# Performance work log

Hardware: AMD Instinct MI355X
Metric: run time of the kernel (lower is better)

Reference implementation:

```python
import jax, jax.numpy as jnp
import numpy as np

B, C, D, L, H = 128, 1000, 300, 40, 100


def setup_inputs() -> dict:
    key = jax.random.key(0)
    ks = jax.random.split(key, 16)
    def rn(i, shape, sc=1.0):
        return (jax.random.normal(ks[i], shape, jnp.float32) * sc).astype(jnp.float32)
    return {
        "utt": rn(0, (B, L, D)),
        "sys_slots": rn(1, (B, D), 0.1),
        "conf_slots": rn(2, (B, D), 0.1),
        "conf_values": rn(3, (B, D), 0.1),
        "y_past_state": jax.random.uniform(ks[4], (B, C), jnp.float32),
        "slot_emb": rn(5, (C, D), 0.1),
        "value_emb": rn(6, (C, D), 0.1),
        "Wc": rn(7, (D, 2 * D), 0.05), "bc": jnp.zeros((D,), jnp.float32),
        "conv_w1": rn(8, (D, D, 1), 0.05), "conv_b1": jnp.zeros((D,), jnp.float32),
        "conv_w2": rn(9, (D, D, 2), 0.05), "conv_b2": jnp.zeros((D,), jnp.float32),
        "conv_w3": rn(10, (D, D, 3), 0.05), "conv_b3": jnp.zeros((D,), jnp.float32),
        "Wd": rn(11, (H, D), 0.05), "bd": jnp.zeros((H,), jnp.float32),
        "Wmr": rn(12, (H, D), 0.05), "bmr": jnp.zeros((H,), jnp.float32),
        "Wmc": rn(13, (H, D), 0.05), "bmc": jnp.zeros((H,), jnp.float32),
        "Wj": rn(14, (1, H), 0.05), "bj": jnp.zeros((1,), jnp.float32),
    }


def _conv_relu_pool(x_ncl, w, b):
    # x_ncl: [B, D, L]; w: [F, D, k] -> relu(conv) then global max-pool over time -> [B, F]
    y = jax.lax.conv_general_dilated(x_ncl, w, (1,), 'VALID',
                                     dimension_numbers=('NCH', 'OIH', 'NCH'))
    y = jax.nn.relu(y + b[None, :, None])
    return jnp.max(y, axis=2)


def _sig_linear(x, W, b):
    # Sequential(Sigmoid, Linear): Linear applied to sigmoid(x)
    return jax.nn.sigmoid(x) @ W.T + b


def reference(utt, sys_slots, conf_slots, conf_values, y_past_state,
              slot_emb, value_emb, Wc, bc,
              conv_w1, conv_b1, conv_w2, conv_b2, conv_w3, conv_b3,
              Wd, bd, Wmr, bmr, Wmc, bmc, Wj, bj):
    # CNN utterance encoder: sum of 3 conv branches (filter widths 1,2,3)
    x = jnp.transpose(utt, (0, 2, 1))  # [B, D, L]
    final_utt = (_conv_relu_pool(x, conv_w1, conv_b1)
                 + _conv_relu_pool(x, conv_w2, conv_b2)
                 + _conv_relu_pool(x, conv_w3, conv_b3))  # [B, D]

    # candidates_transform = sigmoid(Linear(cat(slot_emb, value_emb)))
    cand = jax.nn.sigmoid(jnp.concatenate([slot_emb, value_emb], axis=1) @ Wc.T + bc)  # [C, D]

    # fused version of the per-batch repeat/addcmul loop: [B, C, D]
    contrib = cand[None, :, :] * final_utt[:, None, :]

    y1 = _sig_linear(_sig_linear(contrib, Wd, bd), Wj, bj)  # [B, C, 1]

    # system-act request gate: ([C,D]@[D,B]) @ [B,D] -> [C, D]
    m_r = (slot_emb @ sys_slots.T) @ final_utt
    y2 = _sig_linear(_sig_linear(m_r, Wmr, bmr), Wj, bj)  # [C, 1]

    # system-act confirm gate
    m_c = ((slot_emb @ conf_slots.T) * (value_emb @ conf_values.T)) @ final_utt  # [C, D]
    y3 = _sig_linear(_sig_linear(m_c, Wmc, bmc), Wj, bj)  # [C, 1]

    y_presoftmax = y1 + y2[None, :, :] + y3[None, :, :]  # [B, C, 1]
    combine = 0.5
    return combine * y_presoftmax[..., 0] + (1.0 - combine) * y_past_state  # [B, C]
```

## Files before the change

### kernel.cpp

```cpp
#include <hip/hip_runtime.h>
#include <hip/hip_bf16.h>

#define OFF_Y23     0
#define OFF_BDP     4096
#define OFF_WJP     4544
#define OFF_BCP     4992
#define OFF_BMRP    6272
#define OFF_BMCP    6720
#define OFF_WALLT   7168
#define OFF_PBF     1235968
#define OFF_FUBF    20896768
#define OFF_FUBFT   20978688
#define OFF_CATSV   21060608
#define OFF_WCPK    22371328
#define OFF_CANDBF  22780928
#define OFF_WDFRAG  23436288
#define OFF_WMRFRAG 23507968
#define OFF_WMCFRAG 23579648
#define OFF_SYSB    23651328
#define OFF_CONFSB  23733248
#define OFF_CONFVB  23815168
#define OFF_PRBF    23897088
#define OFF_PCBF    24159232
#define OFF_SMRBF   24421376
#define OFF_SMCBF   25076736
#define OFF_XBF     25732096

typedef short bf16x8_t __attribute__((ext_vector_type(8)));
typedef float f32x4_t  __attribute__((ext_vector_type(4)));

__device__ __forceinline__ float sigmoidf_fast(float x) {
    return __builtin_amdgcn_rcpf(1.0f + __expf(-x));
}
__device__ __forceinline__ unsigned short f2bf(float x) {
    unsigned int u = __float_as_uint(x);
    unsigned int r = (u + 0x7FFFu + ((u >> 16) & 1u)) >> 16;
    return (unsigned short)r;
}
__device__ __forceinline__ float bf2f(unsigned short h) {
    return __uint_as_float(((unsigned int)h) << 16);
}

__device__ __forceinline__ float frag_fetch(const float* __restrict__ W, int i) {
    int entry = i >> 3, e = i & 7;
    int kt = entry / 448;
    int r = entry - kt * 448;
    int ni = r >> 6, lane = r & 63;
    int j = ni * 16 + (lane & 15);
    int k = kt * 32 + (lane >> 4) * 8 + e;
    return (j < 100 && k < 300) ? W[j * 300 + k] : 0.0f;
}

__global__ void pack_kernel(const float* __restrict__ w1, const float* __restrict__ w2,
                            const float* __restrict__ w3, const float* __restrict__ Wc,
                            const float* __restrict__ Wd, const float* __restrict__ Wmr,
                            const float* __restrict__ Wmc, const float* __restrict__ sys,
                            const float* __restrict__ confs, const float* __restrict__ confv,
                            const float* __restrict__ bd, const float* __restrict__ Wj,
                            const float* __restrict__ bmr, const float* __restrict__ bmc,
                            const float* __restrict__ bc, const float* __restrict__ slot,
                            const float* __restrict__ value, const float* __restrict__ utt,
                            unsigned short* __restrict__ WallTbf,
                            unsigned short* __restrict__ WdFrag,
                            unsigned short* __restrict__ WmrFrag,
                            unsigned short* __restrict__ WmcFrag,
                            float* __restrict__ bdPad, float* __restrict__ WjPad,
                            float* __restrict__ bmrPad, float* __restrict__ bmcPad,
                            float* __restrict__ bcPad,
                            unsigned short* __restrict__ sysB,
                            unsigned short* __restrict__ confsB,
                            unsigned short* __restrict__ confvB,
                            unsigned short* __restrict__ catsv,
                            unsigned short* __restrict__ WcPk,
                            unsigned short* __restrict__ Xbf) {
    int idx = blockIdx.x * blockDim.x + threadIdx.x;
    if (idx < 614400) {
        int tap = idx / 102400;
        int rem = idx - tap * 102400;
        int f = rem / 320, k = rem % 320;
        float v = 0.0f;
        if (f < 300 && k < 300) {
            int fd = f * 300 + k;
            if (tap == 0)      v = w1[fd];
            else if (tap == 1) v = w2[fd * 2 + 0];
            else if (tap == 2) v = w2[fd * 2 + 1];
            else               v = w3[fd * 3 + (tap - 3)];
        }
        WallTbf[idx] = f2bf(v);
    } else if (idx < 650240) {
        int i = idx - 614400;
        WdFrag[i] = f2bf(frag_fetch(Wd, i));
    } else if (idx < 686080) {
        int i = idx - 650240;
        WmrFrag[i] = f2bf(frag_fetch(Wmr, i));
    } else if (idx < 721920) {
        int i = idx - 686080;
        WmcFrag[i] = f2bf(frag_fetch(Wmc, i));
    } else if (idx < 722032) {
        int j = idx - 721920; bdPad[j] = (j < 100) ? bd[j] : 0.0f;
    } else if (idx < 722144) {
        int j = idx - 722032; WjPad[j] = (j < 100) ? Wj[j] : 0.0f;
    } else if (idx < 722256) {
        int j = idx - 722144; bmrPad[j] = (j < 100) ? bmr[j] : 0.0f;
    } else if (idx < 722368) {
        int j = idx - 722256; bmcPad[j] = (j < 100) ? bmc[j] : 0.0f;
    } else if (idx < 722688) {
        int j = idx - 722368; bcPad[j] = (j < 300) ? bc[j] : 0.0f;
    } else if (idx < 845568) {
        int i = idx - 722688;
        int m = i / 40960, r = i % 40960;
        int b = r / 320, k = r % 320;
        const float* src = (m == 0) ? sys : ((m == 1) ? confs : confv);
        unsigned short* dst = (m == 0) ? sysB : ((m == 1) ? confsB : confvB);
        dst[r] = f2bf((k < 300) ? src[b * 300 + k] : 0.0f);
    } else if (idx < 1500928) {
        int i = idx - 845568;
        int c = i / 640, k = i % 640;
        float v = 0.0f;
        if (c < 1000) {
            if (k < 300)                   v = slot[c * 300 + k];
            else if (k >= 320 && k < 620)  v = value[c * 300 + (k - 320)];
        }
        catsv[i] = f2bf(v);
    } else if (idx < 1705728) {
        int i = idx - 1500928;
        int f = i / 640, k = i % 640;
        float v = 0.0f;
        if (f < 300) {
            if (k < 300)                   v = Wc[f * 600 + k];
            else if (k >= 320 && k < 620)  v = Wc[f * 600 + 300 + (k - 320)];
        }
        WcPk[i] = f2bf(v);
    } else if (idx < 3344128) {
        int i = idx - 1705728;
        int m = i / 320, k = i % 320;
        Xbf[i] = f2bf((k < 300) ? utt[m * 300 + k] : 0.0f);
    }
}

__global__ __launch_bounds__(256) void early_kernel(
        const unsigned short* __restrict__ Xbf, const unsigned short* __restrict__ WallTbf,
        unsigned short* __restrict__ Pbf,
        const unsigned short* __restrict__ catsv, const unsigned short* __restrict__ WcPk,
        const float* __restrict__ bcPad, unsigned short* __restrict__ candbf,
        const unsigned short* __restrict__ sysB, const unsigned short* __restrict__ confsB,
        const unsigned short* __restrict__ confvB,
        unsigned short* __restrict__ Prbf, unsigned short* __restrict__ Pcbf) {
    __shared__ __attribute__((aligned(16))) char smem[40960];
    const int bid = blockIdx.x;
    const int tid = threadIdx.x;
    const int lane = tid & 63, w = tid >> 6;
    const int ln = lane & 15, lq = lane >> 4;

    if (bid < 600) {
        short* As = (short*)smem;
        short* Bs = (short*)(smem + 10240);
        const int m0 = (bid / 15) * 128;
        const int n0 = (bid % 15) * 128;
        const int wrow = w >> 1, wcol = w & 1;
        f32x4_t acc[4][4];
        #pragma unroll
        for (int i = 0; i < 4; i++)
            #pragma unroll
            for (int j = 0; j < 4; j++) acc[i][j] = (f32x4_t){0.f, 0.f, 0.f, 0.f};
        for (int kk = 0; kk < 320; kk += 32) {
            #pragma unroll
            for (int i = tid; i < 512; i += 256) {
                int row = i >> 2, q = i & 3;
                *(uint4*)(&As[row * 40 + q * 8]) =
                    *(const uint4*)(Xbf + (m0 + row) * 320 + kk + q * 8);
            }
            #pragma unroll
            for (int i = tid; i < 512; i += 256) {
                int row = i >> 2, q = i & 3;
                *(uint4*)(&Bs[row * 40 + q * 8]) =
                    *(const uint4*)(WallTbf + (n0 + row) * 320 + kk + q * 8);
            }
            __syncthreads();
            bf16x8_t a[4], b[4];
            #pragma unroll
            for (int mi = 0; mi < 4; mi++)
                a[mi] = *(const bf16x8_t*)(&As[(wrow * 64 + mi * 16 + ln) * 40 + lq * 8]);
            #pragma unroll
            for (int ni = 0; ni < 4; ni++)
                b[ni] = *(const bf16x8_t*)(&Bs[(wcol * 64 + ni * 16 + ln) * 40 + lq * 8]);
            #pragma unroll
            for (int mi = 0; mi < 4; mi++)
                #pragma unroll
                for (int ni = 0; ni < 4; ni++)
                    acc[mi][ni] = __builtin_amdgcn_mfma_f32_16x16x32_bf16(a[mi], b[ni], acc[mi][ni], 0, 0, 0);
            __syncthreads();
        }
        #pragma unroll
        for (int mi = 0; mi < 4; mi++) {
            #pragma unroll
            for (int ni = 0; ni < 4; ni++) {
                int col = n0 + wcol * 64 + ni * 16 + ln;
                #pragma unroll
                for (int reg = 0; reg < 4; reg++) {
                    int row = m0 + wrow * 64 + mi * 16 + lq * 4 + reg;
                    Pbf[row * 1920 + col] = f2bf(acc[mi][ni][reg]);
                }
            }
        }
    } else if (bid < 680) {
        short* As = (short*)smem;
        short* Bs = (short*)(smem + 5120);
        const int idx2 = bid - 600;
        const int m0 = (idx2 / 5) * 64, n0 = (idx2 % 5) * 64;
        const int wr = w & 1, wc = w >> 1;
        f32x4_t acc[2][2];
        #pragma unroll
        for (int i = 0; i < 2; i++)
            #pragma unroll
            for (int j = 0; j < 2; j++) acc[i][j] = (f32x4_t){0.f, 0.f, 0.f, 0.f};
        const int srow = tid >> 2, sq = tid & 3;
        for (int kk = 0; kk < 640; kk += 32) {
            *(uint4*)(&As[srow * 40 + sq * 8]) = *(const uint4*)(catsv + (m0 + srow) * 640 + kk + sq * 8);
            *(uint4*)(&Bs[srow * 40 + sq * 8]) = *(const uint4*)(WcPk  + (n0 + srow) * 640 + kk + sq * 8);
            __syncthreads();
            bf16x8_t a[2], b[2];
            #pragma unroll
            for (int mi = 0; mi < 2; mi++)
                a[mi] = *(const bf16x8_t*)(&As[(wr * 32 + mi * 16 + ln) * 40 + lq * 8]);
            #pragma unroll
            for (int ni = 0; ni < 2; ni++)
                b[ni] = *(const bf16x8_t*)(&Bs[(wc * 32 + ni * 16 + ln) * 40 + lq * 8]);
            #pragma unroll
            for (int mi = 0; mi < 2; mi++)
                #pragma unroll
                for (int ni = 0; ni < 2; ni++)
                    acc[mi][ni] = __builtin_amdgcn_mfma_f32_16x16x32_bf16(a[mi], b[ni], acc[mi][ni], 0, 0, 0);
            __syncthreads();
        }
        #pragma unroll
        for (int mi = 0; mi < 2; mi++) {
            #pragma unroll
            for (int ni = 0; ni < 2; ni++) {
                int n = n0 + wc * 32 + ni * 16 + ln;
                float bcv = bcPad[n];
                #pragma unroll
                for (int reg = 0; reg < 4; reg++) {
                    int cr = m0 + wr * 32 + mi * 16 + lq * 4 + reg;
                    candbf[cr * 320 + n] = f2bf(sigmoidf_fast(acc[mi][ni][reg] + bcv));
                }
            }
        }
    } else {
        short* As0 = (short*)smem;
        short* As1 = (short*)(smem + 5120);
        short* Bs0 = (short*)(smem + 10240);
        short* Bs1 = (short*)(smem + 20480);
        short* Bs2 = (short*)(smem + 30720);
        const int c0 = (bid - 680) * 64;
        f32x4_t accR[8], accS[8], accV[8];
        #pragma unroll
        for (int i = 0; i < 8; i++) {
            accR[i] = (f32x4_t){0.f, 0.f, 0.f, 0.f};
            accS[i] = (f32x4_t){0.f, 0.f, 0.f, 0.f};
            accV[i] = (f32x4_t){0.f, 0.f, 0.f, 0.f};
        }
        for (int kk = 0; kk < 320; kk += 32) {
            #pragma unroll
            for (int i = tid; i < 512; i += 256) {
                int mat = i >> 8, r2 = i & 255;
                int row = r2 >> 2, q = r2 & 3;
                short* dst = mat ? As1 : As0;
                *(uint4*)(&dst[row * 40 + q * 8]) =
                    *(const uint4*)(catsv + (c0 + row) * 640 + mat * 320 + kk + q * 8);
            }
            #pragma unroll
            for (int i = tid; i < 1536; i += 256) {
                int mat = i >> 9, r2 = i & 511;
                int row = r2 >> 2, q = r2 & 3;
                const unsigned short* src = (mat == 0) ? sysB : ((mat == 1) ? confsB : confvB);
                short* dst = (mat == 0) ? Bs0 : ((mat == 1) ? Bs1 : Bs2);
                *(uint4*)(&dst[row * 40 + q * 8]) =
                    *(const uint4*)(src + row * 320 + kk + q * 8);
            }
            __syncthreads();
            bf16x8_t aS = *(const bf16x8_t*)(&As0[(w * 16 + ln) * 40 + lq * 8]);
            bf16x8_t aV = *(const bf16x8_t*)(&As1[(w * 16 + ln) * 40 + lq * 8]);
            #pragma unroll
            for (int ni = 0; ni < 8; ni++) {
                bf16x8_t bR = *(const bf16x8_t*)(&Bs0[(ni * 16 + ln) * 40 + lq * 8]);
                bf16x8_t bS = *(const bf16x8_t*)(&Bs1[(ni * 16 + ln) * 40 + lq * 8]);
                bf16x8_t bV = *(const bf16x8_t*)(&Bs2[(ni * 16 + ln) * 40 + lq * 8]);
                accR[ni] = __builtin_amdgcn_mfma_f32_16x16x32_bf16(aS, bR, accR[ni], 0, 0, 0);
                accS[ni] = __builtin_amdgcn_mfma_f32_16x16x32_bf16(aS, bS, accS[ni], 0, 0, 0);
                accV[ni] = __builtin_amdgcn_mfma_f32_16x16x32_bf16(aV, bV, accV[ni], 0, 0, 0);
            }
            __syncthreads();
        }
        #pragma unroll
        for (int ni = 0; ni < 8; ni++) {
            int b = ni * 16 + ln;
            #pragma unroll
            for (int reg = 0; reg < 4; reg++) {
                int c = c0 + w * 16 + lq * 4 + reg;
                Prbf[c * 128 + b] = f2bf(accR[ni][reg]);
                Pcbf[c * 128 + b] = f2bf(accS[ni][reg] * accV[ni][reg]);
            }
        }
    }
}

__global__ __launch_bounds__(64) void combine_kernel(const unsigned short* __restrict__ Pbf,
        const float* __restrict__ b1, const float* __restrict__ b2,
        const float* __restrict__ b3, unsigned short* __restrict__ fubf,
        unsigned short* __restrict__ fubfT) {
    int b = blockIdx.x;
    int f = blockIdx.y * 64 + threadIdx.x;
    if (f >= 300) { fubf[b * 320 + f] = 0; fubfT[f * 128 + b] = 0; return; }
    const unsigned short* base = Pbf + (size_t)b * 40 * 1920;
    float m1 = -1e30f, m2 = -1e30f, m3 = -1e30f;
    float p1prev = 0.f, p3prev = 0.f, p3prev2 = 0.f, p4prev = 0.f;
    for (int t = 0; t < 40; ++t) {
        const unsigned short* r = base + t * 1920;
        float p0 = bf2f(r[f]);
        float p1 = bf2f(r[320 + f]);
        float p2 = bf2f(r[640 + f]);
        float p3 = bf2f(r[960 + f]);
        float p4 = bf2f(r[1280 + f]);
        float p5 = bf2f(r[1600 + f]);
        m1 = fmaxf(m1, p0);
        if (t >= 1) m2 = fmaxf(m2, p1prev + p2);
        if (t >= 2) m3 = fmaxf(m3, p3prev2 + p4prev + p5);
        p3prev2 = p3prev; p3prev = p3; p4prev = p4; p1prev = p1;
    }
    float r = fmaxf(m1 + b1[f], 0.f) + fmaxf(m2 + b2[f], 0.f) + fmaxf(m3 + b3[f], 0.f);
    unsigned short rb = f2bf(r);
    fubf[b * 320 + f]  = rb;
    fubfT[f * 128 + b] = rb;
}

__global__ __launch_bounds__(256) void mgate_gemm(const unsigned short* __restrict__ Prbf,
        const unsigned short* __restrict__ Pcbf, const unsigned short* __restrict__ fubfT,
        unsigned short* __restrict__ smrbf, unsigned short* __restrict__ smcbf) {
    __shared__ __attribute__((aligned(16))) short As[2][64 * 40];
    __shared__ __attribute__((aligned(16))) short Bs[64 * 40];
    const int tid = threadIdx.x;
    const int m0 = blockIdx.x * 64, n0 = blockIdx.y * 64;
    const int lane = tid & 63, w = tid >> 6;
    const int wr = w & 1, wc = w >> 1;
    const int ln = lane & 15, lq = lane >> 4;
    f32x4_t accR[2][2], accC[2][2];
    #pragma unroll
    for (int i = 0; i < 2; i++)
        #pragma unroll
        for (int j = 0; j < 2; j++) {
            accR[i][j] = (f32x4_t){0.f, 0.f, 0.f, 0.f};
            accC[i][j] = (f32x4_t){0.f, 0.f, 0.f, 0.f};
        }
    for (int kk = 0; kk < 128; kk += 32) {
        #pragma unroll
        for (int i = tid; i < 512; i += 256) {
            int mat = i >> 8, r2 = i & 255;
            int row = r2 >> 2, q = r2 & 3;
            const unsigned short* src = mat ? Pcbf : Prbf;
            *(uint4*)(&As[mat][row * 40 + q * 8]) =
                *(const uint4*)(src + (m0 + row) * 128 + kk + q * 8);
        }
        if (tid < 256) {
            int row = tid >> 2, q = tid & 3;
            *(uint4*)(&Bs[row * 40 + q * 8]) =
                *(const uint4*)(fubfT + (n0 + row) * 128 + kk + q * 8);
        }
        __syncthreads();
        bf16x8_t aR[2], aC[2], b[2];
        #pragma unroll
        for (int mi = 0; mi < 2; mi++) {
            aR[mi] = *(const bf16x8_t*)(&As[0][(wr * 32 + mi * 16 + ln) * 40 + lq * 8]);
            aC[mi] = *(const bf16x8_t*)(&As[1][(wr * 32 + mi * 16 + ln) * 40 + lq * 8]);
        }
        #pragma unroll
        for (int ni = 0; ni < 2; ni++)
            b[ni] = *(const bf16x8_t*)(&Bs[(wc * 32 + ni * 16 + ln) * 40 + lq * 8]);
        #pragma unroll
        for (int mi = 0; mi < 2; mi++)
            #pragma unroll
            for (int ni = 0; ni < 2; ni++) {
                accR[mi][ni] = __builtin_amdgcn_mfma_f32_16x16x32_bf16(aR[mi], b[ni], accR[mi][ni], 0, 0, 0);
                accC[mi][ni] = __builtin_amdgcn_mfma_f32_16x16x32_bf16(aC[mi], b[ni], accC[mi][ni], 0, 0, 0);
            }
        __syncthreads();
    }
    #pragma unroll
    for (int mi = 0; mi < 2; mi++) {
        #pragma unroll
        for (int ni = 0; ni < 2; ni++) {
            int f = n0 + wc * 32 + ni * 16 + ln;
            #pragma unroll
            for (int reg = 0; reg < 4; reg++) {
                int c = m0 + wr * 32 + mi * 16 + lq * 4 + reg;
                smrbf[c * 320 + f] = f2bf(sigmoidf_fast(accR[mi][ni][reg]));
                smcbf[c * 320 + f] = f2bf(sigmoidf_fast(accC[mi][ni][reg]));
            }
        }
    }
}

__global__ __launch_bounds__(256) void ygate_gemm(const unsigned short* __restrict__ smrbf,
        const unsigned short* __restrict__ smcbf, const unsigned short* __restrict__ WmrFrag,
        const unsigned short* __restrict__ WmcFrag, const float* __restrict__ bmrPad,
        const float* __restrict__ bmcPad, const float* __restrict__ WjPad,
        const float* __restrict__ bj, float* __restrict__ y23) {
    __shared__ __attribute__((aligned(16))) short As[2][64 * 40];
    __shared__ __attribute__((aligned(16))) short Bs[2][3584];
    const int tid = threadIdx.x;
    const int c0 = blockIdx.x * 64;
    const int lane = tid & 63, w = tid >> 6;
    const int ln = lane & 15, lq = lane >> 4;
    f32x4_t accR[7], accC[7];
    #pragma unroll
    for (int i = 0; i < 7; i++) {
        accR[i] = (f32x4_t){0.f, 0.f, 0.f, 0.f};
        accC[i] = (f32x4_t){0.f, 0.f, 0.f, 0.f};
    }
    for (int kt = 0; kt < 10; kt++) {
        int kk = kt * 32;
        #pragma unroll
        for (int i = tid; i < 512; i += 256) {
            int mat = i >> 8, r2 = i & 255;
            int row = r2 >> 2, q = r2 & 3;
            const unsigned short* src = mat ? smcbf : smrbf;
            *(uint4*)(&As[mat][row * 40 + q * 8]) =
                *(const uint4*)(src + (c0 + row) * 320 + kk + q * 8);
        }
        #pragma unroll
        for (int i = tid; i < 896; i += 256) {
            int mat = i / 448, j = i - mat * 448;
            const uint4* s = (const uint4*)((mat ? WmcFrag : WmrFrag) + kt * 3584);
            ((uint4*)&Bs[mat][0])[j] = s[j];
        }
        __syncthreads();
        bf16x8_t aR = *(const bf16x8_t*)(&As[0][(w * 16 + ln) * 40 + lq * 8]);
        bf16x8_t aC = *(const bf16x8_t*)(&As[1][(w * 16 + ln) * 40 + lq * 8]);
        #pragma unroll
        for (int ni = 0; ni < 7; ni++) {
            bf16x8_t bR = *(const bf16x8_t*)(&Bs[0][(ni * 64 + lane) * 8]);
            bf16x8_t bC = *(const bf16x8_t*)(&Bs[1][(ni * 64 + lane) * 8]);
            accR[ni] = __builtin_amdgcn_mfma_f32_16x16x32_bf16(aR, bR, accR[ni], 0, 0, 0);
            accC[ni] = __builtin_amdgcn_mfma_f32_16x16x32_bf16(aC, bC, accC[ni], 0, 0, 0);
        }
        __syncthreads();
    }
    float psum[4] = {0.f, 0.f, 0.f, 0.f};
    #pragma unroll
    for (int ni = 0; ni < 7; ni++) {
        int n = ni * 16 + ln;
        float wj = WjPad[n], br = bmrPad[n], bcv = bmcPad[n];
        #pragma unroll
        for (int reg = 0; reg < 4; reg++) {
            float hr = sigmoidf_fast(accR[ni][reg] + br);
            float hc = sigmoidf_fast(accC[ni][reg] + bcv);
            psum[reg] += (hr + hc) * wj;
        }
    }
    #pragma unroll
    for (int reg = 0; reg < 4; reg++) {
        float v = psum[reg];
        v += __shfl_xor(v, 1);
        v += __shfl_xor(v, 2);
        v += __shfl_xor(v, 4);
        v += __shfl_xor(v, 8);
        if (ln == 0) {
            int c = c0 + w * 16 + lq * 4 + reg;
            y23[c] = v + 2.0f * bj[0];
        }
    }
}

__global__ __launch_bounds__(256) void gemm2_kernel(const unsigned short* __restrict__ candbf,
        const unsigned short* __restrict__ fubf, const unsigned short* __restrict__ WdFrag,
        const float* __restrict__ bdPad, const float* __restrict__ WjPad,
        const float* __restrict__ bj, const float* __restrict__ y23,
        const float* __restrict__ ypast, float* __restrict__ out) {
    __shared__ __attribute__((aligned(16))) short Bs[2][3584];
    __shared__ float bdS[112], WjS[112], ybuf[128];
    const int c = blockIdx.x;
    const int tid = threadIdx.x;
    const int lane = tid & 63, w = tid >> 6;
    const int ln = lane & 15, lq = lane >> 4;
    if (tid < 112) { bdS[tid] = bdPad[tid]; WjS[tid] = WjPad[tid]; }

    const unsigned short* candRow = candbf + c * 320;
    const unsigned short* fuR0 = fubf + (w * 32 + ln) * 320;
    const unsigned short* fuR1 = fuR0 + 16 * 320;

    f32x4_t acc[2][7];
    #pragma unroll
    for (int mi = 0; mi < 2; mi++)
        #pragma unroll
        for (int ni = 0; ni < 7; ni++) acc[mi][ni] = (f32x4_t){0.f, 0.f, 0.f, 0.f};

    {
        const uint4* src = (const uint4*)(WdFrag);
        uint4* dst = (uint4*)&Bs[0][0];
        dst[tid] = src[tid];
        if (tid < 192) dst[tid + 256] = src[tid + 256];
    }
    __syncthreads();

    #pragma unroll
    for (int kt = 0; kt < 10; kt++) {
        if (kt < 9) {
            const uint4* src = (const uint4*)(WdFrag + (kt + 1) * 3584);
            uint4* dst = (uint4*)&Bs[(kt + 1) & 1][0];
            dst[tid] = src[tid];
            if (tid < 192) dst[tid + 256] = src[tid + 256];
        }
        const int k0 = kt * 32 + lq * 8;
        bf16x8_t cf  = *(const bf16x8_t*)(candRow + k0);
        bf16x8_t f0v = *(const bf16x8_t*)(fuR0 + k0);
        bf16x8_t f1v = *(const bf16x8_t*)(fuR1 + k0);
        bf16x8_t a0, a1;
        #pragma unroll
        for (int e = 0; e < 8; e += 2) {
            float cv0 = bf2f((unsigned short)cf[e]);
            float cv1 = bf2f((unsigned short)cf[e + 1]);
            float2 s0 = make_float2(sigmoidf_fast(cv0 * bf2f((unsigned short)f0v[e])),
                                    sigmoidf_fast(cv1 * bf2f((unsigned short)f0v[e + 1])));
            float2 s1 = make_float2(sigmoidf_fast(cv0 * bf2f((unsigned short)f1v[e])),
                                    sigmoidf_fast(cv1 * bf2f((unsigned short)f1v[e + 1])));
            __hip_bfloat162 p0 = __float22bfloat162_rn(s0);
            __hip_bfloat162 p1 = __float22bfloat162_rn(s1);
            ((unsigned int*)&a0)[e >> 1] = *(unsigned int*)&p0;
            ((unsigned int*)&a1)[e >> 1] = *(unsigned int*)&p1;
        }
        #pragma unroll
        for (int ni = 0; ni < 7; ni++) {
            bf16x8_t bfr = *(const bf16x8_t*)(&Bs[kt & 1][(ni * 64 + lane) * 8]);
            acc[0][ni] = __builtin_amdgcn_mfma_f32_16x16x32_bf16(a0, bfr, acc[0][ni], 0, 0, 0);
            acc[1][ni] = __builtin_amdgcn_mfma_f32_16x16x32_bf16(a1, bfr, acc[1][ni], 0, 0, 0);
        }
        __syncthreads();
    }

    float psum[2][4] = {{0.f, 0.f, 0.f, 0.f}, {0.f, 0.f, 0.f, 0.f}};
    #pragma unroll
    for (int mi = 0; mi < 2; mi++) {
        #pragma unroll
        for (int ni = 0; ni < 7; ni++) {
            int n = ni * 16 + ln;
            float bdv = bdS[n], wjv = WjS[n];
            #pragma unroll
            for (int reg = 0; reg < 4; reg++) {
                float h = sigmoidf_fast(acc[mi][ni][reg] + bdv);
                psum[mi][reg] += h * wjv;
            }
        }
    }
    #pragma unroll
    for (int mi = 0; mi < 2; mi++) {
        #pragma unroll
        for (int reg = 0; reg < 4; reg++) {
            float v = psum[mi][reg];
            v += __shfl_xor(v, 1);
            v += __shfl_xor(v, 2);
            v += __shfl_xor(v, 4);
            v += __shfl_xor(v, 8);
            if (ln == 0) ybuf[w * 32 + mi * 16 + lq * 4 + reg] = v;
        }
    }
    __syncthreads();
    if (tid < 128) {
        int b = tid;
        float y1 = ybuf[b] + bj[0];
        out[b * 1000 + c] = 0.5f * (y1 + y23[c]) + 0.5f * ypast[b * 1000 + c];
    }
}

extern "C" void kernel_launch(void* const* d_in, const int* in_sizes, int n_in,
                              void* d_out, int out_size, void* d_ws, size_t ws_size,
                              hipStream_t stream) {
    const float* utt   = (const float*)d_in[0];
    const float* sys   = (const float*)d_in[1];
    const float* confs = (const float*)d_in[2];
    const float* confv = (const float*)d_in[3];
    const float* ypast = (const float*)d_in[4];
    const float* slot  = (const float*)d_in[5];
    const float* value = (const float*)d_in[6];
    const float* Wc    = (const float*)d_in[7];
    const float* bc    = (const float*)d_in[8];
    const float* w1    = (const float*)d_in[9];
    const float* b1    = (const float*)d_in[10];
    const float* w2    = (const float*)d_in[11];
    const float* b2    = (const float*)d_in[12];
    const float* w3    = (const float*)d_in[13];
    const float* b3    = (const float*)d_in[14];
    const float* Wd    = (const float*)d_in[15];
    const float* bd    = (const float*)d_in[16];
    const float* Wmr   = (const float*)d_in[17];
    const float* bmr   = (const float*)d_in[18];
    const float* Wmc   = (const float*)d_in[19];
    const float* bmc   = (const float*)d_in[20];
    const float* Wj    = (const float*)d_in[21];
    const float* bj    = (const float*)d_in[22];

    char* wsb = (char*)d_ws;
    float* y23    = (float*)(wsb + OFF_Y23);
    float* bdPad  = (float*)(wsb + OFF_BDP);
    float* WjPad  = (float*)(wsb + OFF_WJP);
    float* bcPad  = (float*)(wsb + OFF_BCP);
    float* bmrPad = (float*)(wsb + OFF_BMRP);
    float* bmcPad = (float*)(wsb + OFF_BMCP);
    unsigned short* WallTbf = (unsigned short*)(wsb + OFF_WALLT);
    unsigned short* Pbf     = (unsigned short*)(wsb + OFF_PBF);
    unsigned short* fubf    = (unsigned short*)(wsb + OFF_FUBF);
    unsigned short* fubfT   = (unsigned short*)(wsb + OFF_FUBFT);
    unsigned short* catsv   = (unsigned short*)(wsb + OFF_CATSV);
    unsigned short* WcPk    = (unsigned short*)(wsb + OFF_WCPK);
    unsigned short* candbf  = (unsigned short*)(wsb + OFF_CANDBF);
    unsigned short* WdFrag  = (unsigned short*)(wsb + OFF_WDFRAG);
    unsigned short* WmrFrag = (unsigned short*)(wsb + OFF_WMRFRAG);
    unsigned short* WmcFrag = (unsigned short*)(wsb + OFF_WMCFRAG);
    unsigned short* sysB    = (unsigned short*)(wsb + OFF_SYSB);
    unsigned short* confsB  = (unsigned short*)(wsb + OFF_CONFSB);
    unsigned short* confvB  = (unsigned short*)(wsb + OFF_CONFVB);
    unsigned short* Prbf    = (unsigned short*)(wsb + OFF_PRBF);
    unsigned short* Pcbf    = (unsigned short*)(wsb + OFF_PCBF);
    unsigned short* smrbf   = (unsigned short*)(wsb + OFF_SMRBF);
    unsigned short* smcbf   = (unsigned short*)(wsb + OFF_SMCBF);
    unsigned short* Xbf     = (unsigned short*)(wsb + OFF_XBF);
    float* out = (float*)d_out;

    pack_kernel<<<13063, 256, 0, stream>>>(w1, w2, w3, Wc, Wd, Wmr, Wmc, sys, confs, confv,
                                           bd, Wj, bmr, bmc, bc, slot, value, utt,
                                           WallTbf, WdFrag, WmrFrag, WmcFrag,
                                           bdPad, WjPad, bmrPad, bmcPad, bcPad,
                                           sysB, confsB, confvB, catsv, WcPk, Xbf);
    early_kernel<<<696, 256, 0, stream>>>(Xbf, WallTbf, Pbf,
                                          catsv, WcPk, bcPad, candbf,
                                          sysB, confsB, confvB, Prbf, Pcbf);
    combine_kernel<<<dim3(128, 5), 64, 0, stream>>>(Pbf, b1, b2, b3, fubf, fubfT);
    mgate_gemm<<<dim3(16, 5), 256, 0, stream>>>(Prbf, Pcbf, fubfT, smrbf, smcbf);
    ygate_gemm<<<16, 256, 0, stream>>>(smrbf, smcbf, WmrFrag, WmcFrag,
                                       bmrPad, bmcPad, WjPad, bj, y23);
    gemm2_kernel<<<1000, 256, 0, stream>>>(candbf, fubf, WdFrag, bdPad, WjPad,
                                           bj, y23, ypast, out);
}
```

Before: 206.1 us.

## Shrink early_kernel tiles, add register prefetch, reorder blocks for XCD locality

The conv GEMM tile in early_kernel shrinks from 128x128 to 64x128 and gains register-staged prefetch of the next K slice, so global loads overlap the MFMA work. Blocks are remapped so each XCD handles a contiguous range of M rows. The gate-product branch is split into two batch halves. The small cand/gate blocks now come first in the grid, and LDS drops from 40960 to 25600 bytes with a 4-blocks-per-CU launch bound. The aim is more blocks, higher occupancy and better latency hiding, at the cost of more B-tile reloads and extra barriers.

New measurement: 192.6 us. 1.07x faster.

```diff
diff --git a/kernel.cpp b/kernel.cpp
--- a/kernel.cpp
+++ b/kernel.cpp
@@ -138,7 +138,7 @@
     }
 }
 
-__global__ __launch_bounds__(256) void early_kernel(
+__global__ __launch_bounds__(256, 4) void early_kernel(
         const unsigned short* __restrict__ Xbf, const unsigned short* __restrict__ WallTbf,
         unsigned short* __restrict__ Pbf,
         const unsigned short* __restrict__ catsv, const unsigned short* __restrict__ WcPk,
@@ -146,68 +146,82 @@
         const unsigned short* __restrict__ sysB, const unsigned short* __restrict__ confsB,
         const unsigned short* __restrict__ confvB,
         unsigned short* __restrict__ Prbf, unsigned short* __restrict__ Pcbf) {
-    __shared__ __attribute__((aligned(16))) char smem[40960];
+    __shared__ __attribute__((aligned(16))) char smem[25600];
     const int bid = blockIdx.x;
     const int tid = threadIdx.x;
     const int lane = tid & 63, w = tid >> 6;
     const int ln = lane & 15, lq = lane >> 4;
 
-    if (bid < 600) {
+    if (bid >= 112) {
         short* As = (short*)smem;
-        short* Bs = (short*)(smem + 10240);
-        const int m0 = (bid / 15) * 128;
-        const int n0 = (bid % 15) * 128;
-        const int wrow = w >> 1, wcol = w & 1;
-        f32x4_t acc[4][4];
+        short* Bs = (short*)(smem + 5120);
+        const int g = bid - 112;
+        const int xcd = g & 7;
+        const int idx2 = g >> 3;
+        const int m0 = (xcd * 10 + idx2 / 15) * 64;
+        const int n0 = (idx2 % 15) * 128;
+        const int arow = tid >> 2, aq = tid & 3;
+        f32x4_t acc[4][2];
         #pragma unroll
         for (int i = 0; i < 4; i++)
             #pragma unroll
-            for (int j = 0; j < 4; j++) acc[i][j] = (f32x4_t){0.f, 0.f, 0.f, 0.f};
-        for (int kk = 0; kk < 320; kk += 32) {
-            #pragma unroll
-            for (int i = tid; i < 512; i += 256) {
-                int row = i >> 2, q = i & 3;
-                *(uint4*)(&As[row * 40 + q * 8]) =
-                    *(const uint4*)(Xbf + (m0 + row) * 320 + kk + q * 8);
-            }
-            #pragma unroll
-            for (int i = tid; i < 512; i += 256) {
-                int row = i >> 2, q = i & 3;
-                *(uint4*)(&Bs[row * 40 + q * 8]) =
-                    *(const uint4*)(WallTbf + (n0 + row) * 320 + kk + q * 8);
-            }
-            __syncthreads();
-            bf16x8_t a[4], b[4];
+            for (int j = 0; j < 2; j++) acc[i][j] = (f32x4_t){0.f, 0.f, 0.f, 0.f};
+
+        const unsigned short* aSrc  = Xbf + (m0 + arow) * 320 + aq * 8;
+        const unsigned short* bSrc0 = WallTbf + (n0 + arow) * 320 + aq * 8;
+        const unsigned short* bSrc1 = WallTbf + (n0 + 64 + arow) * 320 + aq * 8;
+        uint4 pa  = *(const uint4*)(aSrc);
+        uint4 pb0 = *(const uint4*)(bSrc0);
+        uint4 pb1 = *(const uint4*)(bSrc1);
+        *(uint4*)(&As[arow * 40 + aq * 8]) = pa;
+        *(uint4*)(&Bs[arow * 40 + aq * 8]) = pb0;
+        *(uint4*)(&Bs[(64 + arow) * 40 + aq * 8]) = pb1;
+        __syncthreads();
+
+        #pragma unroll 1
+        for (int kt = 0; kt < 10; kt++) {
+            if (kt < 9) {
+                int kk2 = (kt + 1) * 32;
+                pa  = *(const uint4*)(aSrc + kk2);
+                pb0 = *(const uint4*)(bSrc0 + kk2);
+                pb1 = *(const uint4*)(bSrc1 + kk2);
+            }
+            bf16x8_t a[4], b[2];
             #pragma unroll
             for (int mi = 0; mi < 4; mi++)
-                a[mi] = *(const bf16x8_t*)(&As[(wrow * 64 + mi * 16 + ln) * 40 + lq * 8]);
-            #pragma unroll
-            for (int ni = 0; ni < 4; ni++)
-                b[ni] = *(const bf16x8_t*)(&Bs[(wcol * 64 + ni * 16 + ln) * 40 + lq * 8]);
+                a[mi] = *(const bf16x8_t*)(&As[(mi * 16 + ln) * 40 + lq * 8]);
+            #pragma unroll
+            for (int ni = 0; ni < 2; ni++)
+                b[ni] = *(const bf16x8_t*)(&Bs[(w * 32 + ni * 16 + ln) * 40 + lq * 8]);
             #pragma unroll
             for (int mi = 0; mi < 4; mi++)
                 #pragma unroll
-                for (int ni = 0; ni < 4; ni++)
+                for (int ni = 0; ni < 2; ni++)
                     acc[mi][ni] = __builtin_amdgcn_mfma_f32_16x16x32_bf16(a[mi], b[ni], acc[mi][ni], 0, 0, 0);
-            __syncthreads();
+            if (kt < 9) {
+                __syncthreads();
+                *(uint4*)(&As[arow * 40 + aq * 8]) = pa;
+                *(uint4*)(&Bs[arow * 40 + aq * 8]) = pb0;
+                *(uint4*)(&Bs[(64 + arow) * 40 + aq * 8]) = pb1;
+                __syncthreads();
+            }
         }
         #pragma unroll
         for (int mi = 0; mi < 4; mi++) {
             #pragma unroll
-            for (int ni = 0; ni < 4; ni++) {
-                int col = n0 + wcol * 64 + ni * 16 + ln;
+            for (int ni = 0; ni < 2; ni++) {
+                int col = n0 + w * 32 + ni * 16 + ln;
                 #pragma unroll
                 for (int reg = 0; reg < 4; reg++) {
-                    int row = m0 + wrow * 64 + mi * 16 + lq * 4 + reg;
+                    int row = m0 + mi * 16 + lq * 4 + reg;
                     Pbf[row * 1920 + col] = f2bf(acc[mi][ni][reg]);
                 }
             }
         }
-    } else if (bid < 680) {
+    } else if (bid < 80) {
         short* As = (short*)smem;
         short* Bs = (short*)(smem + 5120);
-        const int idx2 = bid - 600;
-        const int m0 = (idx2 / 5) * 64, n0 = (idx2 % 5) * 64;
+        const int m0 = (bid / 5) * 64, n0 = (bid % 5) * 64;
         const int wr = w & 1, wc = w >> 1;
         f32x4_t acc[2][2];
         #pragma unroll
@@ -250,12 +264,14 @@
         short* As0 = (short*)smem;
         short* As1 = (short*)(smem + 5120);
         short* Bs0 = (short*)(smem + 10240);
-        short* Bs1 = (short*)(smem + 20480);
-        short* Bs2 = (short*)(smem + 30720);
-        const int c0 = (bid - 680) * 64;
-        f32x4_t accR[8], accS[8], accV[8];
-        #pragma unroll
-        for (int i = 0; i < 8; i++) {
+        short* Bs1 = (short*)(smem + 15360);
+        short* Bs2 = (short*)(smem + 20480);
+        const int pid = bid - 80;
+        const int c0 = (pid >> 1) * 64;
+        const int bh = (pid & 1) * 64;
+        f32x4_t accR[4], accS[4], accV[4];
+        #pragma unroll
+        for (int i = 0; i < 4; i++) {
             accR[i] = (f32x4_t){0.f, 0.f, 0.f, 0.f};
             accS[i] = (f32x4_t){0.f, 0.f, 0.f, 0.f};
             accV[i] = (f32x4_t){0.f, 0.f, 0.f, 0.f};
@@ -270,19 +286,19 @@
                     *(const uint4*)(catsv + (c0 + row) * 640 + mat * 320 + kk + q * 8);
             }
             #pragma unroll
-            for (int i = tid; i < 1536; i += 256) {
-                int mat = i >> 9, r2 = i & 511;
+            for (int i = tid; i < 768; i += 256) {
+                int mat = i >> 8, r2 = i & 255;
                 int row = r2 >> 2, q = r2 & 3;
                 const unsigned short* src = (mat == 0) ? sysB : ((mat == 1) ? confsB : confvB);
                 short* dst = (mat == 0) ? Bs0 : ((mat == 1) ? Bs1 : Bs2);
                 *(uint4*)(&dst[row * 40 + q * 8]) =
-                    *(const uint4*)(src + row * 320 + kk + q * 8);
+                    *(const uint4*)(src + (bh + row) * 320 + kk + q * 8);
             }
             __syncthreads();
             bf16x8_t aS = *(const bf16x8_t*)(&As0[(w * 16 + ln) * 40 + lq * 8]);
             bf16x8_t aV = *(const bf16x8_t*)(&As1[(w * 16 + ln) * 40 + lq * 8]);
             #pragma unroll
-            for (int ni = 0; ni < 8; ni++) {
+            for (int ni = 0; ni < 4; ni++) {
                 bf16x8_t bR = *(const bf16x8_t*)(&Bs0[(ni * 16 + ln) * 40 + lq * 8]);
                 bf16x8_t bS = *(const bf16x8_t*)(&Bs1[(ni * 16 + ln) * 40 + lq * 8]);
                 bf16x8_t bV = *(const bf16x8_t*)(&Bs2[(ni * 16 + ln) * 40 + lq * 8]);
@@ -293,8 +309,8 @@
             __syncthreads();
         }
         #pragma unroll
-        for (int ni = 0; ni < 8; ni++) {
-            int b = ni * 16 + ln;
+        for (int ni = 0; ni < 4; ni++) {
+            int b = bh + ni * 16 + ln;
             #pragma unroll
             for (int reg = 0; reg < 4; reg++) {
                 int c = c0 + w * 16 + lq * 4 + reg;
@@ -630,9 +646,9 @@
                                            WallTbf, WdFrag, WmrFrag, WmcFrag,
                                            bdPad, WjPad, bmrPad, bmcPad, bcPad,
                                            sysB, confsB, confvB, catsv, WcPk, Xbf);
-    early_kernel<<<696, 256, 0, stream>>>(Xbf, WallTbf, Pbf,
-                                          catsv, WcPk, bcPad, candbf,
-                                          sysB, confsB, confvB, Prbf, Pcbf);
+    early_kernel<<<1312, 256, 0, stream>>>(Xbf, WallTbf, Pbf,
+                                           catsv, WcPk, bcPad, candbf,
+                                           sysB, confsB, confvB, Prbf, Pcbf);
     combine_kernel<<<dim3(128, 5), 64, 0, stream>>>(Pbf, b1, b2, b3, fubf, fubfT);
     mgate_gemm<<<dim3(16, 5), 256, 0, stream>>>(Prbf, Pcbf, fubfT, smrbf, smcbf);
     ygate_gemm<<<16, 256, 0, stream>>>(smrbf, smcbf, WmrFrag, WmcFrag,
```
